# Kernel tuning notes

Hardware: AMD Instinct MI355X
Metric: run time of the kernel (lower is better)

## Reference

```python
import jax, jax.numpy as jnp
import numpy as np

B, S, D_MODEL, H = 4, 2048, 1024, 16
HD = D_MODEL // H  # head dim = 64


def setup_inputs() -> dict:
    key = jax.random.key(0)
    k1, k2, k3, k4 = jax.random.split(key, 4)
    x = jax.random.normal(k1, (B, S, D_MODEL), dtype=jnp.float32)
    # weights stored as [d_in, d_out] so projection is x @ W
    scale = 1.0 / np.sqrt(D_MODEL)
    Wq = jax.random.normal(k2, (D_MODEL, D_MODEL), dtype=jnp.float32) * scale
    Wk = jax.random.normal(k3, (D_MODEL, D_MODEL), dtype=jnp.float32) * scale
    Wv = jax.random.normal(k4, (D_MODEL, D_MODEL), dtype=jnp.float32) * scale
    return {"x": x, "Wq": Wq, "Wk": Wk, "Wv": Wv}


def reference(x, Wq, Wk, Wv):
    b, s, d_in = x.shape
    h, hd = H, HD
    # project and split heads -> [b, h, s, hd]
    q = (x @ Wq).reshape(b, s, h, hd).transpose(0, 2, 1, 3)
    k = (x @ Wk).reshape(b, s, h, hd).transpose(0, 2, 1, 3)
    v = (x @ Wv).reshape(b, s, h, hd).transpose(0, 2, 1, 3)
    # raw scores [b, h, s, s]; causal mask (strict upper triangle -> -inf)
    scores = jnp.einsum("bhqd,bhkd->bhqk", q, k)
    causal = jnp.tril(jnp.ones((s, s), dtype=bool))
    scores = jnp.where(causal, scores, -jnp.inf)
    attn = jax.nn.softmax(scores / jnp.sqrt(jnp.float32(hd)), axis=-1)
    ctx = jnp.einsum("bhqk,bhkd->bhqd", attn, v)
    return ctx.transpose(0, 2, 1, 3).reshape(b, s, h * hd)
```

## Files before the change

kernel.cpp:

```cpp
#include <hip/hip_runtime.h>

typedef unsigned short u16;
typedef unsigned int u32;
typedef __bf16 bf16_t;
typedef bf16_t bf16x8 __attribute__((ext_vector_type(8)));
typedef bf16_t bf16x4_t __attribute__((ext_vector_type(4)));
typedef float f32x4 __attribute__((ext_vector_type(4)));
typedef unsigned short ushort8_t __attribute__((ext_vector_type(8)));

#define S_LEN 2048
#define DM 1024
#define NH 16
#define HDIM 64
#define PSTR 80
#define TSTR 136

__device__ __forceinline__ u16 f2b(float f) {
  u32 u = __builtin_bit_cast(u32, f);
  u32 r = (u + 0x7FFFu + ((u >> 16) & 1u)) >> 16;
  return (u16)r;
}

__device__ __forceinline__ void gload16(const void* g, void* l) {
  __builtin_amdgcn_global_load_lds((const __attribute__((address_space(1))) void*)g,
                                   (__attribute__((address_space(3))) void*)l,
                                   16, 0, 0);
}

__device__ __forceinline__ bf16x8 ld_bf8(const u16* p) {
  return *reinterpret_cast<const bf16x8*>(p);
}

__device__ __forceinline__ void stage_tile256(const u16* __restrict__ base, int stride,
                                              u16* __restrict__ dst, int tid) {
#pragma unroll
  for (int i = 0; i < 2; ++i) {
    int ci = i * 256 + tid;
    int row = ci >> 3, col = ci & 7;
    gload16(base + (size_t)row * stride + ((col ^ (row & 7)) << 3), dst + ci * 8);
  }
}
__device__ __forceinline__ bf16x8 ld_swz64(const u16* lds, int row, int chunk) {
  return ld_bf8(lds + row * 64 + ((chunk ^ (row & 7)) << 3));
}

__device__ __forceinline__ void stage_tile32(const u16* __restrict__ base,
                                             u16* __restrict__ dst, int tid) {
#pragma unroll
  for (int i = 0; i < 2; ++i) {
    int ci = i * 256 + tid;
    int row = ci >> 2, ch = ci & 3;
    gload16(base + (size_t)row * DM + ((ch ^ ((row >> 1) & 3)) << 3), dst + ci * 8);
  }
}
__device__ __forceinline__ bf16x8 ld_swz32(const u16* lds, int row, int chunk) {
  return ld_bf8(lds + row * 32 + ((chunk ^ ((row >> 1) & 3)) << 3));
}

__global__ __launch_bounds__(256) void k_cvt(const float* __restrict__ in, u16* __restrict__ out) {
  int i = (blockIdx.x * 256 + threadIdx.x) * 4;
  float4 v = *reinterpret_cast<const float4*>(in + i);
  ushort4 o = make_ushort4(f2b(v.x), f2b(v.y), f2b(v.z), f2b(v.w));
  *reinterpret_cast<ushort4*>(out + i) = o;
}

__global__ __launch_bounds__(256) void k_wt(const float* __restrict__ W, u16* __restrict__ Wt) {
  __shared__ float t[32][33];
  int n0 = blockIdx.x * 32, k0 = blockIdx.y * 32;
  int tx = threadIdx.x & 31, ty = threadIdx.x >> 5;
#pragma unroll
  for (int i = 0; i < 32; i += 8)
    t[ty + i][tx] = W[(size_t)(k0 + ty + i) * DM + n0 + tx];
  __syncthreads();
#pragma unroll
  for (int i = 0; i < 32; i += 8)
    Wt[(size_t)(n0 + ty + i) * DM + k0 + tx] = f2b(t[tx][ty + i]);
}

__global__ __launch_bounds__(256) void k_gemm(const u16* __restrict__ Xb, const u16* __restrict__ Wt_all,
                                              u16* __restrict__ Out_all, u16* __restrict__ Vt,
                                              float qscale) {
  __shared__ __attribute__((aligned(16))) u16 smem[128 * TSTR];
  u16* At = smem;
  u16* Bt = smem + 4096;
  int bx = blockIdx.x, by = blockIdx.y;
  int n0g = bx * 128, m0 = by * 128;
  int which = n0g >> 10;
  int n0 = n0g & 1023;
  int tid = threadIdx.x;
  int lane = tid & 63, w = tid >> 6;
  int l15 = lane & 15, lg = lane >> 4;
  int wm = w >> 1, wn = w & 1;

  const u16* Ag = Xb + (size_t)m0 * DM;
  const u16* Bg = Wt_all + (size_t)n0g * DM;

  f32x4 acc[4][4] = {};
  for (int kt = 0; kt < 32; ++kt) {
    int kk = kt * 32;
    stage_tile32(Ag + kk, At, tid);
    stage_tile32(Bg + kk, Bt, tid);
    __syncthreads();
    bf16x8 af[4], bfr[4];
#pragma unroll
    for (int mi = 0; mi < 4; ++mi)
      af[mi] = ld_swz32(At, wm * 64 + mi * 16 + l15, lg);
#pragma unroll
    for (int ni = 0; ni < 4; ++ni)
      bfr[ni] = ld_swz32(Bt, wn * 64 + ni * 16 + l15, lg);
#pragma unroll
    for (int mi = 0; mi < 4; ++mi)
#pragma unroll
      for (int ni = 0; ni < 4; ++ni)
        acc[mi][ni] = __builtin_amdgcn_mfma_f32_16x16x32_bf16(af[mi], bfr[ni], acc[mi][ni], 0, 0, 0);
    __syncthreads();
  }

  if (which < 2) {
    float scale = (which == 0) ? qscale : 1.0f;
    u16* Out = Out_all + (size_t)which * (size_t)(4 * NH * S_LEN * HDIM);
#pragma unroll
    for (int mi = 0; mi < 4; ++mi) {
#pragma unroll
      for (int ni = 0; ni < 4; ++ni) {
#pragma unroll
        for (int r = 0; r < 4; ++r) {
          int m = m0 + wm * 64 + mi * 16 + lg * 4 + r;
          int n = n0 + wn * 64 + ni * 16 + l15;
          int b = m >> 11, s = m & 2047;
          int h = n >> 6, hd = n & 63;
          Out[(((size_t)(b * NH + h)) * S_LEN + s) * HDIM + hd] = f2b(acc[mi][ni][r] * scale);
        }
      }
    }
  } else {
    u16* T = smem;
#pragma unroll
    for (int mi = 0; mi < 4; ++mi) {
#pragma unroll
      for (int ni = 0; ni < 4; ++ni) {
        ushort4 w4 = make_ushort4(f2b(acc[mi][ni][0]), f2b(acc[mi][ni][1]),
                                  f2b(acc[mi][ni][2]), f2b(acc[mi][ni][3]));
        *reinterpret_cast<ushort4*>(T + (wn * 64 + ni * 16 + l15) * TSTR +
                                    wm * 64 + mi * 16 + lg * 4) = w4;
      }
    }
    __syncthreads();
    int base_h = n0 >> 6;
    int b = m0 >> 11, s0 = m0 & 2047;
#pragma unroll
    for (int pass = 0; pass < 8; ++pass) {
      int row = pass * 16 + (tid >> 4);
      int col = (tid & 15) * 8;
      ushort8_t v = *reinterpret_cast<const ushort8_t*>(T + row * TSTR + col);
      int h = base_h + (row >> 6), hd = row & 63;
      *reinterpret_cast<ushort8_t*>(Vt + ((size_t)((b * NH + h) * HDIM + hd)) * S_LEN + s0 + col) = v;
    }
  }
}

__device__ __forceinline__ void attn_strip(const u16* __restrict__ Qp, const u16* __restrict__ Kp,
                                           const u16* __restrict__ Vp, float* __restrict__ out,
                                           int b, int h, int qbase, int w, int tid, int lane, int nt,
                                           u16 (*Kd)[64 * 64], u16* __restrict__ Vd,
                                           u16* __restrict__ Pw) {
  int l15 = lane & 15, lg = lane >> 4;
  int qrow = qbase + w * 16;
  bf16x8 qf0 = ld_bf8(Qp + (size_t)(qrow + l15) * HDIM + lg * 8);
  bf16x8 qf1 = ld_bf8(Qp + (size_t)(qrow + l15) * HDIM + 32 + lg * 8);
  f32x4 o[4] = {};
  float ls = 0.f;
  int qa = qrow + l15;

  stage_tile256(Kp, HDIM, Kd[0], tid);
  asm volatile("s_waitcnt vmcnt(0)" ::: "memory");
  __builtin_amdgcn_sched_barrier(0);
  __builtin_amdgcn_s_barrier();
  __builtin_amdgcn_sched_barrier(0);

  for (int kt = 0; kt < nt; ++kt) {
    int k0 = kt * 64;
    int cur = kt & 1;
    bool pre = (kt + 1 < nt);
    stage_tile256(Vp + k0, S_LEN, Vd, tid);
    if (pre) stage_tile256(Kp + (size_t)(k0 + 64) * HDIM, HDIM, Kd[cur ^ 1], tid);

    if (pre) asm volatile("s_waitcnt vmcnt(4)" ::: "memory");
    else     asm volatile("s_waitcnt vmcnt(2)" ::: "memory");
    __builtin_amdgcn_sched_barrier(0);
    __builtin_amdgcn_s_barrier();
    __builtin_amdgcn_sched_barrier(0);

    f32x4 sc[4];
    __builtin_amdgcn_s_setprio(1);
#pragma unroll
    for (int kb = 0; kb < 4; ++kb) {
      bf16x8 kf0 = ld_swz64(Kd[cur], kb * 16 + l15, lg);
      bf16x8 kf1 = ld_swz64(Kd[cur], kb * 16 + l15, 4 + lg);
      f32x4 z = {};
      z = __builtin_amdgcn_mfma_f32_16x16x32_bf16(kf0, qf0, z, 0, 0, 0);
      sc[kb] = __builtin_amdgcn_mfma_f32_16x16x32_bf16(kf1, qf1, sc[kb] = z, 0, 0, 0);
    }
    __builtin_amdgcn_s_setprio(0);

    if (kt == nt - 1) {
#pragma unroll
      for (int kb = 0; kb < 4; ++kb) {
        bf16x4_t pw;
#pragma unroll
        for (int r = 0; r < 4; ++r) {
          int key = k0 + kb * 16 + lg * 4 + r;
          float e = __builtin_amdgcn_exp2f(sc[kb][r]);
          e = (key > qa) ? 0.f : e;
          ls += e;
          pw[r] = (bf16_t)e;
        }
        *reinterpret_cast<bf16x4_t*>(Pw + l15 * PSTR + kb * 16 + lg * 4) = pw;
      }
    } else {
#pragma unroll
      for (int kb = 0; kb < 4; ++kb) {
        bf16x4_t pw;
#pragma unroll
        for (int r = 0; r < 4; ++r) {
          float e = __builtin_amdgcn_exp2f(sc[kb][r]);
          ls += e;
          pw[r] = (bf16_t)e;
        }
        *reinterpret_cast<bf16x4_t*>(Pw + l15 * PSTR + kb * 16 + lg * 4) = pw;
      }
    }
    asm volatile("" ::: "memory");
    bf16x8 pf0 = ld_bf8(Pw + l15 * PSTR + lg * 8);
    bf16x8 pf1 = ld_bf8(Pw + l15 * PSTR + 32 + lg * 8);

    if (pre) asm volatile("s_waitcnt vmcnt(2) lgkmcnt(0)" ::: "memory");
    else     asm volatile("s_waitcnt vmcnt(0) lgkmcnt(0)" ::: "memory");
    __builtin_amdgcn_sched_barrier(0);
    __builtin_amdgcn_s_barrier();
    __builtin_amdgcn_sched_barrier(0);

    __builtin_amdgcn_s_setprio(1);
#pragma unroll
    for (int n = 0; n < 4; ++n) {
      bf16x8 vf0 = ld_swz64(Vd, n * 16 + l15, lg);
      bf16x8 vf1 = ld_swz64(Vd, n * 16 + l15, 4 + lg);
      o[n] = __builtin_amdgcn_mfma_f32_16x16x32_bf16(pf0, vf0, o[n], 0, 0, 0);
      o[n] = __builtin_amdgcn_mfma_f32_16x16x32_bf16(pf1, vf1, o[n], 0, 0, 0);
    }
    __builtin_amdgcn_s_setprio(0);

    __builtin_amdgcn_sched_barrier(0);
    __builtin_amdgcn_s_barrier();
    __builtin_amdgcn_sched_barrier(0);
  }

  ls += __shfl_xor(ls, 16);
  ls += __shfl_xor(ls, 32);
  float l0 = __shfl(ls, lg * 4 + 0);
  float l1 = __shfl(ls, lg * 4 + 1);
  float l2 = __shfl(ls, lg * 4 + 2);
  float l3 = __shfl(ls, lg * 4 + 3);
  float lsr[4] = {l0, l1, l2, l3};
#pragma unroll
  for (int r = 0; r < 4; ++r) {
    float inv = 1.f / lsr[r];
    int row = qrow + lg * 4 + r;
#pragma unroll
    for (int n = 0; n < 4; ++n)
      out[((size_t)b * S_LEN + row) * DM + h * HDIM + n * 16 + l15] = o[n][r] * inv;
  }
}

__global__ __launch_bounds__(256, 4) void k_attn(const u16* __restrict__ Qb, const u16* __restrict__ Kb,
                                                 const u16* __restrict__ Vtb, float* __restrict__ out) {
  __shared__ u16 Kd[2][64 * 64];
  __shared__ u16 Vd[64 * 64];
  __shared__ u16 Plds[4][16 * PSTR];
  int j = blockIdx.x;
  int m = j >> 3;
  int x = m & 15;
  int bh = (j & 7) + 8 * (m >> 4);
  int tid = threadIdx.x, lane = tid & 63, w = tid >> 6;
  int b = bh >> 4, h = bh & 15;
  const u16* Qp = Qb + (size_t)bh * S_LEN * HDIM;
  const u16* Kp = Kb + (size_t)bh * S_LEN * HDIM;
  const u16* Vp = Vtb + (size_t)bh * HDIM * S_LEN;
  u16* Pw = Plds[w];
  attn_strip(Qp, Kp, Vp, out, b, h, x * 64, w, tid, lane, x + 1, Kd, Vd, Pw);
  attn_strip(Qp, Kp, Vp, out, b, h, (31 - x) * 64, w, tid, lane, 32 - x, Kd, Vd, Pw);
}

extern "C" void kernel_launch(void* const* d_in, const int* in_sizes, int n_in,
                              void* d_out, int out_size, void* d_ws, size_t ws_size,
                              hipStream_t stream) {
  const float* x  = (const float*)d_in[0];
  const float* Wq = (const float*)d_in[1];
  const float* Wk = (const float*)d_in[2];
  const float* Wv = (const float*)d_in[3];
  float* out = (float*)d_out;

  u16* ws  = (u16*)d_ws;
  u16* xb  = ws;
  u16* wqt = xb + 8388608;
  u16* wkt = wqt + 1048576;
  u16* wvt = wkt + 1048576;
  u16* Qb  = wvt + 1048576;
  u16* Kb  = Qb + 8388608;
  u16* Vtb = Kb + 8388608;

  const float qscale = 0.125f * 1.44269504088896f;

  k_cvt<<<8192, 256, 0, stream>>>(x, xb);
  k_wt<<<dim3(32, 32), 256, 0, stream>>>(Wq, wqt);
  k_wt<<<dim3(32, 32), 256, 0, stream>>>(Wk, wkt);
  k_wt<<<dim3(32, 32), 256, 0, stream>>>(Wv, wvt);
  k_gemm<<<dim3(24, 64), 256, 0, stream>>>(xb, wqt, Qb, Vtb, qscale);
  k_attn<<<1024, 256, 0, stream>>>(Qb, Kb, Vtb, out);
}
```

Before: 145.8 us.

## Stage Q/K GEMM epilogue through LDS for vectorized stores; merge weight transposes

For the Q and K projections, the MFMA operands are swapped so each lane's accumulator holds contiguous head-dim values. The tile is written to LDS and then stored to global memory as 16-byte vectors, replacing scattered 2-byte stores. The three weight-transpose launches are also merged into one 3D-grid launch, which saves launch overhead. This adds an extra LDS round trip and a barrier in the Q/K epilogue.

```diff
diff --git a/kernel.cpp b/kernel.cpp
--- a/kernel.cpp
+++ b/kernel.cpp
@@ -64,8 +64,11 @@
   *reinterpret_cast<ushort4*>(out + i) = o;
 }
 
-__global__ __launch_bounds__(256) void k_wt(const float* __restrict__ W, u16* __restrict__ Wt) {
+__global__ __launch_bounds__(256) void k_wt3(const float* __restrict__ Wq, const float* __restrict__ Wk,
+                                             const float* __restrict__ Wv, u16* __restrict__ Wt) {
   __shared__ float t[32][33];
+  const float* W = (blockIdx.z == 0) ? Wq : (blockIdx.z == 1) ? Wk : Wv;
+  u16* dst = Wt + (size_t)blockIdx.z * (DM * DM);
   int n0 = blockIdx.x * 32, k0 = blockIdx.y * 32;
   int tx = threadIdx.x & 31, ty = threadIdx.x >> 5;
 #pragma unroll
@@ -74,7 +77,7 @@
   __syncthreads();
 #pragma unroll
   for (int i = 0; i < 32; i += 8)
-    Wt[(size_t)(n0 + ty + i) * DM + k0 + tx] = f2b(t[tx][ty + i]);
+    dst[(size_t)(n0 + ty + i) * DM + k0 + tx] = f2b(t[tx][ty + i]);
 }
 
 __global__ __launch_bounds__(256) void k_gemm(const u16* __restrict__ Xb, const u16* __restrict__ Wt_all,
@@ -108,14 +111,24 @@
 #pragma unroll
     for (int ni = 0; ni < 4; ++ni)
       bfr[ni] = ld_swz32(Bt, wn * 64 + ni * 16 + l15, lg);
-#pragma unroll
-    for (int mi = 0; mi < 4; ++mi)
-#pragma unroll
-      for (int ni = 0; ni < 4; ++ni)
-        acc[mi][ni] = __builtin_amdgcn_mfma_f32_16x16x32_bf16(af[mi], bfr[ni], acc[mi][ni], 0, 0, 0);
+    if (which < 2) {
+#pragma unroll
+      for (int mi = 0; mi < 4; ++mi)
+#pragma unroll
+        for (int ni = 0; ni < 4; ++ni)
+          acc[mi][ni] = __builtin_amdgcn_mfma_f32_16x16x32_bf16(bfr[ni], af[mi], acc[mi][ni], 0, 0, 0);
+    } else {
+#pragma unroll
+      for (int mi = 0; mi < 4; ++mi)
+#pragma unroll
+        for (int ni = 0; ni < 4; ++ni)
+          acc[mi][ni] = __builtin_amdgcn_mfma_f32_16x16x32_bf16(af[mi], bfr[ni], acc[mi][ni], 0, 0, 0);
+    }
     __syncthreads();
   }
 
+  u16* T = smem;
+  int b = m0 >> 11, s0 = m0 & 2047;
   if (which < 2) {
     float scale = (which == 0) ? qscale : 1.0f;
     u16* Out = Out_all + (size_t)which * (size_t)(4 * NH * S_LEN * HDIM);
@@ -123,18 +136,23 @@
     for (int mi = 0; mi < 4; ++mi) {
 #pragma unroll
       for (int ni = 0; ni < 4; ++ni) {
-#pragma unroll
-        for (int r = 0; r < 4; ++r) {
-          int m = m0 + wm * 64 + mi * 16 + lg * 4 + r;
-          int n = n0 + wn * 64 + ni * 16 + l15;
-          int b = m >> 11, s = m & 2047;
-          int h = n >> 6, hd = n & 63;
-          Out[(((size_t)(b * NH + h)) * S_LEN + s) * HDIM + hd] = f2b(acc[mi][ni][r] * scale);
-        }
+        ushort4 w4 = make_ushort4(f2b(acc[mi][ni][0] * scale), f2b(acc[mi][ni][1] * scale),
+                                  f2b(acc[mi][ni][2] * scale), f2b(acc[mi][ni][3] * scale));
+        *reinterpret_cast<ushort4*>(T + (wm * 64 + mi * 16 + l15) * TSTR +
+                                    wn * 64 + ni * 16 + lg * 4) = w4;
       }
     }
+    __syncthreads();
+    int base_h = n0 >> 6;
+#pragma unroll
+    for (int pass = 0; pass < 8; ++pass) {
+      int row = pass * 16 + (tid >> 4);
+      int col = (tid & 15) * 8;
+      ushort8_t v = *reinterpret_cast<const ushort8_t*>(T + row * TSTR + col);
+      int h = base_h + (col >> 6), hd = col & 63;
+      *reinterpret_cast<ushort8_t*>(Out + ((size_t)(b * NH + h) * S_LEN + s0 + row) * HDIM + hd) = v;
+    }
   } else {
-    u16* T = smem;
 #pragma unroll
     for (int mi = 0; mi < 4; ++mi) {
 #pragma unroll
@@ -147,7 +165,6 @@
     }
     __syncthreads();
     int base_h = n0 >> 6;
-    int b = m0 >> 11, s0 = m0 & 2047;
 #pragma unroll
     for (int pass = 0; pass < 8; ++pass) {
       int row = pass * 16 + (tid >> 4);
@@ -303,18 +320,14 @@
   u16* ws  = (u16*)d_ws;
   u16* xb  = ws;
   u16* wqt = xb + 8388608;
-  u16* wkt = wqt + 1048576;
-  u16* wvt = wkt + 1048576;
-  u16* Qb  = wvt + 1048576;
+  u16* Qb  = wqt + 3145728;
   u16* Kb  = Qb + 8388608;
   u16* Vtb = Kb + 8388608;
 
   const float qscale = 0.125f * 1.44269504088896f;
 
   k_cvt<<<8192, 256, 0, stream>>>(x, xb);
-  k_wt<<<dim3(32, 32), 256, 0, stream>>>(Wq, wqt);
-  k_wt<<<dim3(32, 32), 256, 0, stream>>>(Wk, wkt);
-  k_wt<<<dim3(32, 32), 256, 0, stream>>>(Wv, wvt);
+  k_wt3<<<dim3(32, 32, 3), 256, 0, stream>>>(Wq, Wk, Wv, wqt);
   k_gemm<<<dim3(24, 64), 256, 0, stream>>>(xb, wqt, Qb, Vtb, qscale);
   k_attn<<<1024, 256, 0, stream>>>(Qb, Kb, Vtb, out);
 }
```

New measurement: 141.6 us. -2.9%, faster.
